# Performance work log

Measured on AMD Instinct MI355X. Metric: run time of the kernel, lower is better.

## Reference

```python
import jax, jax.numpy as jnp
import numpy as np
import math

B, T, D = 2, 2048, 1024
H = 16
DH = D // H  # 64
ROPE_BASE = 10000.0


def _rope_tables(seq_len, d_head, dtype=jnp.float32):
    inv_freq = 1.0 / (ROPE_BASE ** (jnp.arange(0, d_head, 2, dtype=jnp.float32) / d_head))
    pos = jnp.arange(seq_len, dtype=jnp.float32)
    freqs = jnp.outer(pos, inv_freq)            # [T, DH/2]
    emb = jnp.concatenate([freqs, freqs], -1)   # [T, DH]
    return jnp.cos(emb).astype(dtype), jnp.sin(emb).astype(dtype)


def _rotate_half(x):
    half = x.shape[-1] // 2
    return jnp.concatenate([-x[..., half:], x[..., :half]], axis=-1)


def setup_inputs() -> dict:
    key = jax.random.key(0)
    k1, k2, k3 = jax.random.split(key, 3)
    x = jax.random.normal(k1, (B, T, D), dtype=jnp.float32)
    qkv_w = jax.random.normal(k2, (D, 3 * D), dtype=jnp.float32) * (1.0 / math.sqrt(D))
    out_w = jax.random.normal(k3, (D, D), dtype=jnp.float32) * (1.0 / math.sqrt(D))
    out_b = jnp.zeros((D,), dtype=jnp.float32)
    mask = jnp.tril(jnp.ones((T, T), dtype=bool))[None, None]  # causal [1,1,T,T]
    return {"x": x, "mask": mask, "qkv_w": qkv_w, "out_w": out_w, "out_b": out_b}


def reference(x, mask, qkv_w, out_w, out_b):
    Bv, Tv, Dv = x.shape
    qkv = (x @ qkv_w).reshape(Bv, Tv, 3, H, DH)
    # [B, H, T, DH]
    q = jnp.transpose(qkv[:, :, 0], (0, 2, 1, 3))
    k = jnp.transpose(qkv[:, :, 1], (0, 2, 1, 3))
    v = jnp.transpose(qkv[:, :, 2], (0, 2, 1, 3))
    cos, sin = _rope_tables(Tv, DH, x.dtype)
    cos = cos[None, None]  # [1,1,T,DH]
    sin = sin[None, None]
    q = q * cos + _rotate_half(q) * sin
    k = k * cos + _rotate_half(k) * sin
    scores = jnp.einsum('bhqd,bhkd->bhqk', q, k) / math.sqrt(DH)
    scores = jnp.where(mask, scores, -jnp.inf)
    probs = jax.nn.softmax(scores, axis=-1)  # dropout = identity in eval mode
    out = jnp.einsum('bhqk,bhkd->bhqd', probs, v)
    out = jnp.transpose(out, (0, 2, 1, 3)).reshape(Bv, Tv, Dv)
    return out @ out_w + out_b
```

## Files before the change

### kernel.cpp

```cpp
#include <hip/hip_runtime.h>
#include <math.h>

typedef __attribute__((ext_vector_type(8))) short short8;
typedef __attribute__((ext_vector_type(4))) float f32x4;

static __device__ __forceinline__ unsigned short f2bf(float f) {
  unsigned u = __builtin_bit_cast(unsigned, f);
  u += 0x7fffu + ((u >> 16) & 1u);
  return (unsigned short)(u >> 16);
}
static __device__ __forceinline__ float bf2f(unsigned short h) {
  return __builtin_bit_cast(float, ((unsigned)h) << 16);
}
static __device__ __forceinline__ unsigned pack2bf(float a, float b) {
  return (unsigned)f2bf(a) | ((unsigned)f2bf(b) << 16);
}
static __device__ __forceinline__ unsigned pack2bf_t(float a, float b) {
  return __builtin_amdgcn_perm(__builtin_bit_cast(unsigned, b),
                               __builtin_bit_cast(unsigned, a), 0x07060302u);
}

typedef __attribute__((address_space(3))) unsigned short lds_us;
typedef __attribute__((address_space(1))) const unsigned short gbl_us;

static __device__ __forceinline__ void gld_lds16(const unsigned short* g,
                                                 unsigned short* l) {
  __builtin_amdgcn_global_load_lds((gbl_us*)g, (lds_us*)l, 16, 0, 0);
}

__global__ __launch_bounds__(256) void prep(const float* __restrict__ x,
                                            unsigned short* __restrict__ xb,
                                            const float* __restrict__ qkv_w,
                                            unsigned short* __restrict__ wqkvT,
                                            const float* __restrict__ out_w,
                                            unsigned short* __restrict__ woT) {
  __shared__ unsigned short T[64][68];
  const int blk = blockIdx.x;
  if (blk < 2048) {
    int i = (blk * 256 + threadIdx.x) * 8;
    float4 a = *(const float4*)(x + i);
    float4 b = *(const float4*)(x + i + 4);
    ushort4 u0 = {f2bf(a.x), f2bf(a.y), f2bf(a.z), f2bf(a.w)};
    ushort4 u1 = {f2bf(b.x), f2bf(b.y), f2bf(b.z), f2bf(b.w)};
    *(ushort4*)(xb + i) = u0;
    *(ushort4*)(xb + i + 4) = u1;
    return;
  }
  const float* in;
  unsigned short* out;
  int R, C, bx, by;
  if (blk < 2816) {
    in = qkv_w; out = wqkvT; R = 1024; C = 3072;
    bx = (blk - 2048) % 48; by = (blk - 2048) / 48;
  } else {
    in = out_w; out = woT; R = 1024; C = 1024;
    bx = (blk - 2816) % 16; by = (blk - 2816) / 16;
  }
  const int r0 = by * 64, c0 = bx * 64;
  const int tr = threadIdx.x >> 2;
  const int tc = (threadIdx.x & 3) * 16;
#pragma unroll
  for (int j = 0; j < 4; ++j) {
    float4 v = *(const float4*)(in + (size_t)(r0 + tr) * C + c0 + tc + j * 4);
    ushort4 u = {f2bf(v.x), f2bf(v.y), f2bf(v.z), f2bf(v.w)};
    *(ushort4*)&T[tr][tc + j * 4] = u;
  }
  __syncthreads();
  const int oc = tr;
#pragma unroll
  for (int g = 0; g < 4; ++g) {
    ushort4 u;
    u.x = T[tc + g * 4 + 0][oc];
    u.y = T[tc + g * 4 + 1][oc];
    u.z = T[tc + g * 4 + 2][oc];
    u.w = T[tc + g * 4 + 3][oc];
    *(ushort4*)(out + (size_t)(c0 + oc) * R + r0 + tc + g * 4) = u;
  }
}

__global__ __launch_bounds__(512) void gemm_qkv512(
    const unsigned short* __restrict__ A, const unsigned short* __restrict__ BT,
    unsigned short* __restrict__ qo, unsigned short* __restrict__ ko,
    unsigned short* __restrict__ vo) {
  __shared__ unsigned short As[2][4096];
  __shared__ unsigned short Bs[2][4096];
  const int tid = threadIdx.x;
  const int w = tid >> 6;
  const int lane = tid & 63;
  const int l15 = lane & 15;
  const int quad = lane >> 4;
  const int wm = w >> 2;
  const int wn = w & 3;
  const int m0 = blockIdx.y * 128;
  const int n0 = blockIdx.x * 128;

  f32x4 acc[4][2];
  const f32x4 zero4 = {0.f, 0.f, 0.f, 0.f};
#pragma unroll
  for (int mt = 0; mt < 4; ++mt)
#pragma unroll
    for (int nt = 0; nt < 2; ++nt) acc[mt][nt] = zero4;

  const int srow = tid >> 2;
  const int skch = (tid & 3) ^ ((srow >> 1) & 3);
  const int coff = tid * 8;
  const unsigned short* gA = A + (size_t)(m0 + srow) * 1024 + skch * 8;
  const unsigned short* gB = BT + (size_t)(n0 + srow) * 1024 + skch * 8;

  const int swz = (quad ^ ((l15 >> 1) & 3)) * 8;
  int aoff[4], boff[2];
#pragma unroll
  for (int t = 0; t < 4; ++t)
    aoff[t] = (wm * 64 + t * 16 + l15) * 32 + swz;
#pragma unroll
  for (int t = 0; t < 2; ++t)
    boff[t] = ((wn >> 1) * 64 + (wn & 1) * 16 + t * 32 + l15) * 32 + swz;

  auto issue = [&](int k0, int buf) {
    gld_lds16(gA + k0, &As[buf][coff]);
    gld_lds16(gB + k0, &Bs[buf][coff]);
  };

  issue(0, 0);
  for (int it = 0; it < 32; ++it) {
    const int cur = it & 1;
    __syncthreads();
    if (it + 1 < 32) issue((it + 1) * 32, cur ^ 1);

    short8 af[4], bf[2];
#pragma unroll
    for (int t = 0; t < 4; ++t) af[t] = *(const short8*)(&As[cur][aoff[t]]);
#pragma unroll
    for (int t = 0; t < 2; ++t) bf[t] = *(const short8*)(&Bs[cur][boff[t]]);
#pragma unroll
    for (int mt = 0; mt < 4; ++mt)
#pragma unroll
      for (int nt = 0; nt < 2; ++nt)
        acc[mt][nt] =
            __builtin_amdgcn_mfma_f32_16x16x32_bf16(af[mt], bf[nt], acc[mt][nt], 0, 0, 0);
  }

  const int b = m0 >> 11;
  const int ngrp = n0 + (wn >> 1) * 64;
  const int which = ngrp >> 10;
  const int h = (ngrp & 1023) >> 6;
  const int bh = b * 16 + h;
  if (which < 2) {
    unsigned short* dst = which ? ko : qo;
    const float qs = (which == 0) ? 0.1803368801111f : 1.0f;
    const int p = (wn & 1) * 16 + l15;
    float inv = __builtin_amdgcn_exp2f((float)p * -0.41524101186f) *
                0.15915494309f;
#pragma unroll
    for (int mt = 0; mt < 4; ++mt)
#pragma unroll
      for (int r = 0; r < 4; ++r) {
        int t = (m0 + wm * 64 + mt * 16 + quad * 4 + r) & 2047;
        float rv = __builtin_amdgcn_fractf((float)t * inv);
        float s = __builtin_amdgcn_sinf(rv);
        float c = __builtin_amdgcn_cosf(rv);
        float x0 = acc[mt][0][r], x1 = acc[mt][1][r];
        size_t rowoff = ((size_t)bh * 2048 + t) * 64;
        dst[rowoff + p]      = f2bf((x0 * c - x1 * s) * qs);
        dst[rowoff + p + 32] = f2bf((x1 * c + x0 * s) * qs);
      }
  } else {
#pragma unroll
    for (int mt = 0; mt < 4; ++mt) {
      int t0 = (m0 + wm * 64 + mt * 16 + quad * 4) & 2047;
#pragma unroll
      for (int nt = 0; nt < 2; ++nt) {
        int dh = (wn & 1) * 16 + nt * 32 + l15;
        ushort4 st = {f2bf(acc[mt][nt][0]), f2bf(acc[mt][nt][1]),
                      f2bf(acc[mt][nt][2]), f2bf(acc[mt][nt][3])};
        *(ushort4*)(vo + ((size_t)bh * 64 + dh) * 2048 + t0) = st;
      }
    }
  }
}

__global__ __launch_bounds__(256) void gemm_out(
    const unsigned short* __restrict__ A, const unsigned short* __restrict__ BT,
    const float* __restrict__ bias, float* __restrict__ out) {
  __shared__ unsigned short As[2][4096];
  __shared__ unsigned short Bs[2][2048];
  const int tid = threadIdx.x;
  const int w = tid >> 6;
  const int lane = tid & 63;
  const int l15 = lane & 15;
  const int quad = lane >> 4;
  const int wm = w >> 1, wn = w & 1;
  const int m0 = blockIdx.y * 128;
  const int n0 = blockIdx.x * 64;

  f32x4 acc[4][2];
  const f32x4 zero4 = {0.f, 0.f, 0.f, 0.f};
#pragma unroll
  for (int mt = 0; mt < 4; ++mt)
#pragma unroll
    for (int nt = 0; nt < 2; ++nt) acc[mt][nt] = zero4;

  int aco[2];
  const unsigned short* gA[2];
#pragma unroll
  for (int i = 0; i < 2; ++i) {
    int c = i * 256 + w * 64 + lane;
    int srow = c >> 2;
    int skch = (c & 3) ^ ((srow >> 1) & 3);
    aco[i] = c * 8;
    gA[i] = A + (size_t)(m0 + srow) * 1024 + skch * 8;
  }
  const int bc = w * 64 + lane;
  const int bsrow = bc >> 2;
  const int bskch = (bc & 3) ^ ((bsrow >> 1) & 3);
  const int bco = bc * 8;
  const unsigned short* gB = BT + (size_t)(n0 + bsrow) * 1024 + bskch * 8;

  const int swz = (quad ^ ((l15 >> 1) & 3)) * 8;
  int aoff[4], boff[2];
#pragma unroll
  for (int t = 0; t < 4; ++t) aoff[t] = (wm * 64 + t * 16 + l15) * 32 + swz;
#pragma unroll
  for (int t = 0; t < 2; ++t) boff[t] = (wn * 32 + t * 16 + l15) * 32 + swz;

  auto issue = [&](int k0, int buf) {
#pragma unroll
    for (int i = 0; i < 2; ++i) gld_lds16(gA[i] + k0, &As[buf][aco[i]]);
    gld_lds16(gB + k0, &Bs[buf][bco]);
  };

  issue(0, 0);
  for (int it = 0; it < 32; ++it) {
    const int cur = it & 1;
    __syncthreads();
    if (it + 1 < 32) issue((it + 1) * 32, cur ^ 1);

    short8 af[4], bf[2];
#pragma unroll
    for (int t = 0; t < 4; ++t) af[t] = *(const short8*)(&As[cur][aoff[t]]);
#pragma unroll
    for (int t = 0; t < 2; ++t) bf[t] = *(const short8*)(&Bs[cur][boff[t]]);
#pragma unroll
    for (int mt = 0; mt < 4; ++mt)
#pragma unroll
      for (int nt = 0; nt < 2; ++nt)
        acc[mt][nt] =
            __builtin_amdgcn_mfma_f32_16x16x32_bf16(af[mt], bf[nt], acc[mt][nt], 0, 0, 0);
  }

  const int nbase = n0 + wn * 32;
  float bv[2];
#pragma unroll
  for (int nt = 0; nt < 2; ++nt) bv[nt] = bias[nbase + nt * 16 + l15];
#pragma unroll
  for (int mt = 0; mt < 4; ++mt)
#pragma unroll
    for (int r = 0; r < 4; ++r) {
      int m = m0 + wm * 64 + mt * 16 + quad * 4 + r;
      float* orow = out + (size_t)m * 1024 + nbase + l15;
#pragma unroll
      for (int nt = 0; nt < 2; ++nt) orow[nt * 16] = acc[mt][nt][r] + bv[nt];
    }
}

__global__ __launch_bounds__(128, 4) void attn_mfma(
    const unsigned short* __restrict__ qg, const unsigned short* __restrict__ kg,
    const unsigned short* __restrict__ vtg, unsigned short* __restrict__ og,
    unsigned short* __restrict__ OpA,
    unsigned short* __restrict__ OpB,
    float* __restrict__ Lpart) {
  __shared__ unsigned short Ks[2][2048];
  __shared__ unsigned short Vt[2][2048];
  __shared__ unsigned short Ps[2][1024];
  const int bh = blockIdx.x;
  const int slot = blockIdx.y;
  int qb, chunk;
  if (slot < 32) {
    qb = 24 + (slot & 7);
    chunk = slot >> 3;
  } else if (slot < 56) {
    int s = slot - 32;
    qb = 16 + (s & 7);
    chunk = s >> 3;
  } else if (slot < 72) {
    int s = slot - 56;
    qb = 8 + (s & 7);
    chunk = s >> 3;
  } else {
    qb = slot - 72;
    chunk = 0;
  }
  const int n = qb >= 24 ? 4 : (qb >= 16 ? 3 : (qb >= 8 ? 2 : 1));
  const int t0 = chunk * 2 * (qb + 1) / n;
  const int t1 = (chunk + 1) * 2 * (qb + 1) / n;

  const int tid = threadIdx.x;
  const int w = tid >> 6;
  const int lane = tid & 63;
  const int l15 = lane & 15;
  const int quad = lane >> 4;
  const int m7 = l15 & 7;

  const int gq0 = qb * 64;
  const int qw = w * 32;

  short8 qf[2][2];
#pragma unroll
  for (int g = 0; g < 2; ++g) {
    const unsigned short* qrow =
        qg + ((size_t)bh * 2048 + gq0 + qw + g * 16 + l15) * 64;
    qf[g][0] = *(const short8*)(qrow + quad * 8);
    qf[g][1] = *(const short8*)(qrow + quad * 8 + 32);
  }

  f32x4 acc_o[2][4];
  f32x4 acc_l[2];
  const f32x4 zero4 = {0.f, 0.f, 0.f, 0.f};
#pragma unroll
  for (int g = 0; g < 2; ++g) {
    acc_l[g] = zero4;
#pragma unroll
    for (int nt = 0; nt < 4; ++nt) acc_o[g][nt] = zero4;
  }
  const short one_bf = (short)0x3F80;
  const short8 ones8 = {one_bf, one_bf, one_bf, one_bf,
                        one_bf, one_bf, one_bf, one_bf};

  const unsigned short* kbase = kg + (size_t)bh * 2048 * 64;
  const unsigned short* vtbase = vtg + (size_t)bh * 64 * 2048;
  unsigned short* pb = Ps[w];

  int doff[2], koff[2], voff[2];
#pragma unroll
  for (int i = 0; i < 2; ++i) {
    int d = i * 128 + tid;
    doff[i] = d * 8;
    int r = d >> 3;
    int lc = (d & 7) ^ (r & 7);
    koff[i] = r * 64 + lc * 8;
    int dh = (lc >> 2) * 32 + r;
    voff[i] = dh * 2048 + (lc & 3) * 8;
  }

  auto issue = [&](int kb, int buf) {
#pragma unroll
    for (int i = 0; i < 2; ++i) {
      gld_lds16(kbase + kb * 2048 + koff[i], &Ks[buf][doff[i]]);
      gld_lds16(vtbase + voff[i] + kb * 32, &Vt[buf][doff[i]]);
    }
  };

  const int kc0 = ((quad ^ m7) & 7) * 8;
  const int kc1 = kc0 ^ 32;
  int prd[2], vch[2];
#pragma unroll
  for (int g = 0; g < 2; ++g) prd[g] = l15 * 64 + (((g << 2) | quad) ^ m7) * 8;
#pragma unroll
  for (int h = 0; h < 2; ++h) vch[h] = (((h << 2) | quad) ^ m7) * 8;

  issue(t0, 0);
  for (int kb = t0; kb < t1; ++kb) {
    const int cur = (kb - t0) & 1;
    __syncthreads();
    if (kb + 1 < t1) issue(kb + 1, cur ^ 1);

    const unsigned short* kt = Ks[cur];
    const unsigned short* vt = Vt[cur];

    f32x4 s[2][2];
#pragma unroll
    for (int nt = 0; nt < 2; ++nt) {
      const unsigned short* kr = kt + (nt * 16 + l15) * 64;
      short8 kf0 = *(const short8*)(kr + kc0);
      short8 kf1 = *(const short8*)(kr + kc1);
#pragma unroll
      for (int g = 0; g < 2; ++g) {
        f32x4 cc = zero4;
        cc = __builtin_amdgcn_mfma_f32_16x16x32_bf16(kf0, qf[g][0], cc, 0, 0, 0);
        cc = __builtin_amdgcn_mfma_f32_16x16x32_bf16(kf1, qf[g][1], cc, 0, 0, 0);
        s[g][nt] = cc;
      }
    }

    if ((kb >> 1) == qb) {
#pragma unroll
      for (int g = 0; g < 2; ++g) {
        int gq = gq0 + qw + g * 16 + l15;
#pragma unroll
        for (int nt = 0; nt < 2; ++nt) {
          int gk = kb * 32 + nt * 16 + quad * 4;
#pragma unroll
          for (int r = 0; r < 4; ++r)
            if (gk + r > gq) s[g][nt][r] = -INFINITY;
        }
      }
    }

#pragma unroll
    for (int g = 0; g < 2; ++g)
#pragma unroll
      for (int nt = 0; nt < 2; ++nt) {
        float e0 = __builtin_amdgcn_exp2f(s[g][nt][0]);
        float e1 = __builtin_amdgcn_exp2f(s[g][nt][1]);
        float e2 = __builtin_amdgcn_exp2f(s[g][nt][2]);
        float e3 = __builtin_amdgcn_exp2f(s[g][nt][3]);
        int cidx = ((g << 2) | (nt * 2 + (quad >> 1))) ^ m7;
        uint2 pk;
        pk.x = pack2bf_t(e0, e1);
        pk.y = pack2bf_t(e2, e3);
        *(uint2*)&pb[l15 * 64 + cidx * 8 + (quad & 1) * 4] = pk;
      }

    short8 pfa = *(const short8*)&pb[prd[0]];
    short8 pfb = *(const short8*)&pb[prd[1]];

    acc_l[0] = __builtin_amdgcn_mfma_f32_16x16x32_bf16(ones8, pfa, acc_l[0], 0, 0, 0);
    acc_l[1] = __builtin_amdgcn_mfma_f32_16x16x32_bf16(ones8, pfb, acc_l[1], 0, 0, 0);

#pragma unroll
    for (int nt = 0; nt < 4; ++nt) {
      const unsigned short* vr = vt + ((nt & 1) * 16 + l15) * 64 + vch[nt >> 1];
      short8 vf = *(const short8*)vr;
      acc_o[0][nt] = __builtin_amdgcn_mfma_f32_16x16x32_bf16(vf, pfa, acc_o[0][nt], 0, 0, 0);
      acc_o[1][nt] = __builtin_amdgcn_mfma_f32_16x16x32_bf16(vf, pfb, acc_o[1][nt], 0, 0, 0);
    }
  }

  float lsum[2] = {acc_l[0][0], acc_l[1][0]};

  if (n == 1) {
    const int b = bh >> 4;
    const int h = bh & 15;
#pragma unroll
    for (int g = 0; g < 2; ++g) {
      float inv_l = 1.0f / lsum[g];
      unsigned short* orow =
          og + ((size_t)(b * 2048 + gq0 + qw + g * 16 + l15)) * 1024 + h * 64 +
          quad * 4;
#pragma unroll
      for (int nt = 0; nt < 4; ++nt) {
        *(unsigned*)(orow + nt * 16) =
            pack2bf(acc_o[g][nt][0] * inv_l, acc_o[g][nt][1] * inv_l);
        *(unsigned*)(orow + nt * 16 + 2) =
            pack2bf(acc_o[g][nt][2] * inv_l, acc_o[g][nt][3] * inv_l);
      }
    }
  } else {
    const int pidx = (qb < 16) ? (qb - 8) * 2 + chunk
                               : (qb < 24) ? 16 + (qb - 16) * 3 + chunk
                                           : 40 + (qb - 24) * 4 + chunk;
    unsigned short* obase = (pidx < 16)
                                ? OpB + ((size_t)(bh * 16 + pidx)) * 4096
                                : OpA + ((size_t)(bh * 56 + (pidx - 16))) * 4096;
#pragma unroll
    for (int g = 0; g < 2; ++g) {
      unsigned short* orow = obase + (qw + g * 16 + l15) * 64 + quad * 4;
#pragma unroll
      for (int nt = 0; nt < 4; ++nt) {
        *(unsigned*)(orow + nt * 16) = pack2bf(acc_o[g][nt][0], acc_o[g][nt][1]);
        *(unsigned*)(orow + nt * 16 + 2) = pack2bf(acc_o[g][nt][2], acc_o[g][nt][3]);
      }
      if (quad == 0)
        Lpart[(bh * 72 + pidx) * 64 + qw + g * 16 + l15] = lsum[g];
    }
  }
}

__global__ __launch_bounds__(256) void attn_combine(
    const unsigned short* __restrict__ OpA, const unsigned short* __restrict__ OpB,
    const float* __restrict__ Lpart, unsigned short* __restrict__ og) {
  int i = blockIdx.x * 256 + threadIdx.x;
  int dh = (i & 15) * 4;
  int q = (i >> 4) & 63;
  int idx = i >> 10;
  int bh = idx / 24;
  int qr = idx - bh * 24;
  int qb = 8 + qr;
  int count = qr < 8 ? 2 : (qr < 16 ? 3 : 4);
  int pstart = qr < 8 ? qr * 2 : (qr < 16 ? 16 + (qr - 8) * 3 : 40 + (qr - 16) * 4);
  float o0 = 0.f, o1 = 0.f, o2 = 0.f, o3 = 0.f, l = 0.f;
  for (int c = 0; c < count; ++c) {
    int pidx = pstart + c;
    const unsigned short* obase =
        (pidx < 16) ? OpB + ((size_t)(bh * 16 + pidx)) * 4096
                    : OpA + ((size_t)(bh * 56 + (pidx - 16))) * 4096;
    ushort4 a = *(const ushort4*)(obase + q * 64 + dh);
    o0 += bf2f(a.x);
    o1 += bf2f(a.y);
    o2 += bf2f(a.z);
    o3 += bf2f(a.w);
    l += Lpart[(bh * 72 + pidx) * 64 + q];
  }
  float inv = 1.0f / l;
  int bb = bh >> 4, h = bh & 15;
  int t = qb * 64 + q;
  unsigned short* orow = og + ((size_t)(bb * 2048 + t)) * 1024 + h * 64 + dh;
  *(unsigned*)(orow) = pack2bf(o0 * inv, o1 * inv);
  *(unsigned*)(orow + 2) = pack2bf(o2 * inv, o3 * inv);
}

extern "C" void kernel_launch(void* const* d_in, const int* in_sizes, int n_in,
                              void* d_out, int out_size, void* d_ws,
                              size_t ws_size, hipStream_t stream) {
  const float* x = (const float*)d_in[0];
  const float* qkv_w = (const float*)d_in[2];
  const float* out_w = (const float*)d_in[3];
  const float* out_b = (const float*)d_in[4];
  float* out = (float*)d_out;

  unsigned short* xb = (unsigned short*)d_ws;
  unsigned short* wqkvT = xb + 4194304;
  unsigned short* woT = wqkvT + 3145728;
  unsigned short* qb16 = woT + 1048576;
  unsigned short* kb16 = qb16 + 4194304;
  unsigned short* vt16 = kb16 + 4194304;
  unsigned short* ab = vt16 + 4194304;
  unsigned short* OpB = ab + 4194304;
  float* Lpart = (float*)(OpB + 4194304);
  unsigned short* OpA = xb;

  prep<<<3072, 256, 0, stream>>>(x, xb, qkv_w, wqkvT, out_w, woT);
  gemm_qkv512<<<dim3(24, 32), 512, 0, stream>>>(xb, wqkvT, qb16, kb16, vt16);
  attn_mfma<<<dim3(32, 80), 128, 0, stream>>>(qb16, kb16, vt16, ab, OpA, OpB,
                                              Lpart);
  attn_combine<<<3072, 256, 0, stream>>>(OpA, OpB, Lpart, ab);
  gemm_out<<<dim3(16, 32), 256, 0, stream>>>(ab, woT, out_b, out);
}
```

Baseline: 190.4 us.

## Load K/V tiles directly from global into registers, drop LDS staging and barriers

The attention kernel no longer stages K and V^T tiles through double-buffered shared memory with async global-to-LDS loads and a block-wide barrier each iteration. Each wave now loads its K fragments straight into registers, prefetching the next tile one iteration ahead, and loads V fragments directly from global at the top of each iteration. MFMA sections are wrapped in s_setprio raises, and launch bounds drop from 4 to 3 blocks per CU to allow more registers. This removes LDS traffic and __syncthreads, at the cost of redundant global/L2 reads across the waves of a block and exposed V load latency.

Measured after the change: 231.8 us. +21.7%, slower.

```diff
diff --git a/kernel.cpp b/kernel.cpp
--- a/kernel.cpp
+++ b/kernel.cpp
@@ -263,14 +263,12 @@
     }
 }
 
-__global__ __launch_bounds__(128, 4) void attn_mfma(
+__global__ __launch_bounds__(128, 3) void attn_mfma(
     const unsigned short* __restrict__ qg, const unsigned short* __restrict__ kg,
     const unsigned short* __restrict__ vtg, unsigned short* __restrict__ og,
     unsigned short* __restrict__ OpA,
     unsigned short* __restrict__ OpB,
     float* __restrict__ Lpart) {
-  __shared__ unsigned short Ks[2][2048];
-  __shared__ unsigned short Vt[2][2048];
   __shared__ unsigned short Ps[2][1024];
   const int bh = blockIdx.x;
   const int slot = blockIdx.y;
@@ -326,61 +324,49 @@
   const short8 ones8 = {one_bf, one_bf, one_bf, one_bf,
                         one_bf, one_bf, one_bf, one_bf};
 
-  const unsigned short* kbase = kg + (size_t)bh * 2048 * 64;
-  const unsigned short* vtbase = vtg + (size_t)bh * 64 * 2048;
+  const unsigned short* kp =
+      kg + (size_t)bh * 2048 * 64 + l15 * 64 + quad * 8;
+  const unsigned short* vp =
+      vtg + (size_t)bh * 64 * 2048 + (size_t)l15 * 2048 + quad * 8;
   unsigned short* pb = Ps[w];
 
-  int doff[2], koff[2], voff[2];
-#pragma unroll
-  for (int i = 0; i < 2; ++i) {
-    int d = i * 128 + tid;
-    doff[i] = d * 8;
-    int r = d >> 3;
-    int lc = (d & 7) ^ (r & 7);
-    koff[i] = r * 64 + lc * 8;
-    int dh = (lc >> 2) * 32 + r;
-    voff[i] = dh * 2048 + (lc & 3) * 8;
-  }
-
-  auto issue = [&](int kb, int buf) {
-#pragma unroll
-    for (int i = 0; i < 2; ++i) {
-      gld_lds16(kbase + kb * 2048 + koff[i], &Ks[buf][doff[i]]);
-      gld_lds16(vtbase + voff[i] + kb * 32, &Vt[buf][doff[i]]);
+  int prd[2];
+#pragma unroll
+  for (int g = 0; g < 2; ++g) prd[g] = l15 * 64 + (((g << 2) | quad) ^ m7) * 8;
+
+  auto loadK = [&](int kb, short8 (&kf)[2][2]) {
+    const unsigned short* p = kp + kb * 2048;
+#pragma unroll
+    for (int nt = 0; nt < 2; ++nt) {
+      kf[nt][0] = *(const short8*)(p + nt * 1024);
+      kf[nt][1] = *(const short8*)(p + nt * 1024 + 32);
     }
   };
 
-  const int kc0 = ((quad ^ m7) & 7) * 8;
-  const int kc1 = kc0 ^ 32;
-  int prd[2], vch[2];
-#pragma unroll
-  for (int g = 0; g < 2; ++g) prd[g] = l15 * 64 + (((g << 2) | quad) ^ m7) * 8;
-#pragma unroll
-  for (int h = 0; h < 2; ++h) vch[h] = (((h << 2) | quad) ^ m7) * 8;
-
-  issue(t0, 0);
+  short8 kf[2][2], kfn[2][2];
+  loadK(t0, kf);
+
   for (int kb = t0; kb < t1; ++kb) {
-    const int cur = (kb - t0) & 1;
-    __syncthreads();
-    if (kb + 1 < t1) issue(kb + 1, cur ^ 1);
-
-    const unsigned short* kt = Ks[cur];
-    const unsigned short* vt = Vt[cur];
+    short8 vf[4];
+#pragma unroll
+    for (int nt = 0; nt < 4; ++nt)
+      vf[nt] = *(const short8*)(vp + (size_t)nt * 32768 + kb * 32);
 
     f32x4 s[2][2];
+    __builtin_amdgcn_s_setprio(1);
 #pragma unroll
     for (int nt = 0; nt < 2; ++nt) {
-      const unsigned short* kr = kt + (nt * 16 + l15) * 64;
-      short8 kf0 = *(const short8*)(kr + kc0);
-      short8 kf1 = *(const short8*)(kr + kc1);
 #pragma unroll
       for (int g = 0; g < 2; ++g) {
         f32x4 cc = zero4;
-        cc = __builtin_amdgcn_mfma_f32_16x16x32_bf16(kf0, qf[g][0], cc, 0, 0, 0);
-        cc = __builtin_amdgcn_mfma_f32_16x16x32_bf16(kf1, qf[g][1], cc, 0, 0, 0);
+        cc = __builtin_amdgcn_mfma_f32_16x16x32_bf16(kf[nt][0], qf[g][0], cc, 0, 0, 0);
+        cc = __builtin_amdgcn_mfma_f32_16x16x32_bf16(kf[nt][1], qf[g][1], cc, 0, 0, 0);
         s[g][nt] = cc;
       }
     }
+    __builtin_amdgcn_s_setprio(0);
+
+    if (kb + 1 < t1) loadK(kb + 1, kfn);
 
     if ((kb >> 1) == qb) {
 #pragma unroll
@@ -414,15 +400,23 @@
     short8 pfa = *(const short8*)&pb[prd[0]];
     short8 pfb = *(const short8*)&pb[prd[1]];
 
+    __builtin_amdgcn_s_setprio(1);
     acc_l[0] = __builtin_amdgcn_mfma_f32_16x16x32_bf16(ones8, pfa, acc_l[0], 0, 0, 0);
     acc_l[1] = __builtin_amdgcn_mfma_f32_16x16x32_bf16(ones8, pfb, acc_l[1], 0, 0, 0);
 
 #pragma unroll
     for (int nt = 0; nt < 4; ++nt) {
-      const unsigned short* vr = vt + ((nt & 1) * 16 + l15) * 64 + vch[nt >> 1];
-      short8 vf = *(const short8*)vr;
-      acc_o[0][nt] = __builtin_amdgcn_mfma_f32_16x16x32_bf16(vf, pfa, acc_o[0][nt], 0, 0, 0);
-      acc_o[1][nt] = __builtin_amdgcn_mfma_f32_16x16x32_bf16(vf, pfb, acc_o[1][nt], 0, 0, 0);
+      acc_o[0][nt] = __builtin_amdgcn_mfma_f32_16x16x32_bf16(vf[nt], pfa, acc_o[0][nt], 0, 0, 0);
+      acc_o[1][nt] = __builtin_amdgcn_mfma_f32_16x16x32_bf16(vf[nt], pfb, acc_o[1][nt], 0, 0, 0);
+    }
+    __builtin_amdgcn_s_setprio(0);
+
+    if (kb + 1 < t1) {
+#pragma unroll
+      for (int nt = 0; nt < 2; ++nt) {
+        kf[nt][0] = kfn[nt][0];
+        kf[nt][1] = kfn[nt][1];
+      }
     }
   }
 
```

## Widen attention blocks to 128 queries with 4 waves and set MFMA priority

Applied to the files above, without the earlier changes.

The attention kernel now runs 256-thread blocks of four waves, so each block covers a 128-row query tile instead of 64. Each K/V tile staged in LDS is therefore shared by twice as many queries, and each thread issues one async load per tile instead of two. The split-K chunk scheduling, partial-output indexing and combine kernel are remapped to the new tile size. s_setprio hints are placed around the MFMA sections to favour matrix issue. The trade-offs are half as many blocks, which means less parallelism and coarser load balance, plus more LDS per block.

Measured after the change: 196.2 us. +3.1%, slower.

```diff
diff --git a/kernel.cpp b/kernel.cpp
--- a/kernel.cpp
+++ b/kernel.cpp
@@ -263,7 +263,7 @@
     }
 }
 
-__global__ __launch_bounds__(128, 4) void attn_mfma(
+__global__ __launch_bounds__(256, 4) void attn_mfma(
     const unsigned short* __restrict__ qg, const unsigned short* __restrict__ kg,
     const unsigned short* __restrict__ vtg, unsigned short* __restrict__ og,
     unsigned short* __restrict__ OpA,
@@ -271,28 +271,29 @@
     float* __restrict__ Lpart) {
   __shared__ unsigned short Ks[2][2048];
   __shared__ unsigned short Vt[2][2048];
-  __shared__ unsigned short Ps[2][1024];
+  __shared__ unsigned short Ps[4][1024];
   const int bh = blockIdx.x;
   const int slot = blockIdx.y;
-  int qb, chunk;
-  if (slot < 32) {
-    qb = 24 + (slot & 7);
-    chunk = slot >> 3;
-  } else if (slot < 56) {
-    int s = slot - 32;
-    qb = 16 + (s & 7);
-    chunk = s >> 3;
-  } else if (slot < 72) {
-    int s = slot - 56;
-    qb = 8 + (s & 7);
-    chunk = s >> 3;
+  int qb2, chunk;
+  if (slot < 16) {
+    qb2 = 12 + (slot & 3);
+    chunk = slot >> 2;
+  } else if (slot < 28) {
+    int s = slot - 16;
+    qb2 = 8 + (s & 3);
+    chunk = s >> 2;
+  } else if (slot < 36) {
+    int s = slot - 28;
+    qb2 = 4 + (s & 3);
+    chunk = s >> 2;
   } else {
-    qb = slot - 72;
+    qb2 = slot - 36;
     chunk = 0;
   }
-  const int n = qb >= 24 ? 4 : (qb >= 16 ? 3 : (qb >= 8 ? 2 : 1));
-  const int t0 = chunk * 2 * (qb + 1) / n;
-  const int t1 = (chunk + 1) * 2 * (qb + 1) / n;
+  const int n = qb2 >= 12 ? 4 : (qb2 >= 8 ? 3 : (qb2 >= 4 ? 2 : 1));
+  const int tt = 4 * (qb2 + 1);
+  const int t0 = chunk * tt / n;
+  const int t1 = (chunk + 1) * tt / n;
 
   const int tid = threadIdx.x;
   const int w = tid >> 6;
@@ -301,7 +302,7 @@
   const int quad = lane >> 4;
   const int m7 = l15 & 7;
 
-  const int gq0 = qb * 64;
+  const int gq0 = qb2 * 128;
   const int qw = w * 32;
 
   short8 qf[2][2];
@@ -330,24 +331,17 @@
   const unsigned short* vtbase = vtg + (size_t)bh * 64 * 2048;
   unsigned short* pb = Ps[w];
 
-  int doff[2], koff[2], voff[2];
-#pragma unroll
-  for (int i = 0; i < 2; ++i) {
-    int d = i * 128 + tid;
-    doff[i] = d * 8;
-    int r = d >> 3;
-    int lc = (d & 7) ^ (r & 7);
-    koff[i] = r * 64 + lc * 8;
-    int dh = (lc >> 2) * 32 + r;
-    voff[i] = dh * 2048 + (lc & 3) * 8;
-  }
+  const int d = tid;
+  const int doff = d * 8;
+  const int srow = d >> 3;
+  const int slc = (d & 7) ^ (srow & 7);
+  const int koff = srow * 64 + slc * 8;
+  const int sdh = (slc >> 2) * 32 + srow;
+  const int voff = sdh * 2048 + (slc & 3) * 8;
 
   auto issue = [&](int kb, int buf) {
-#pragma unroll
-    for (int i = 0; i < 2; ++i) {
-      gld_lds16(kbase + kb * 2048 + koff[i], &Ks[buf][doff[i]]);
-      gld_lds16(vtbase + voff[i] + kb * 32, &Vt[buf][doff[i]]);
-    }
+    gld_lds16(kbase + kb * 2048 + koff, &Ks[buf][doff]);
+    gld_lds16(vtbase + voff + kb * 32, &Vt[buf][doff]);
   };
 
   const int kc0 = ((quad ^ m7) & 7) * 8;
@@ -368,6 +362,7 @@
     const unsigned short* vt = Vt[cur];
 
     f32x4 s[2][2];
+    __builtin_amdgcn_s_setprio(1);
 #pragma unroll
     for (int nt = 0; nt < 2; ++nt) {
       const unsigned short* kr = kt + (nt * 16 + l15) * 64;
@@ -381,8 +376,9 @@
         s[g][nt] = cc;
       }
     }
-
-    if ((kb >> 1) == qb) {
+    __builtin_amdgcn_s_setprio(0);
+
+    if ((kb >> 2) == qb2) {
 #pragma unroll
       for (int g = 0; g < 2; ++g) {
         int gq = gq0 + qw + g * 16 + l15;
@@ -414,6 +410,7 @@
     short8 pfa = *(const short8*)&pb[prd[0]];
     short8 pfb = *(const short8*)&pb[prd[1]];
 
+    __builtin_amdgcn_s_setprio(1);
     acc_l[0] = __builtin_amdgcn_mfma_f32_16x16x32_bf16(ones8, pfa, acc_l[0], 0, 0, 0);
     acc_l[1] = __builtin_amdgcn_mfma_f32_16x16x32_bf16(ones8, pfb, acc_l[1], 0, 0, 0);
 
@@ -424,6 +421,7 @@
       acc_o[0][nt] = __builtin_amdgcn_mfma_f32_16x16x32_bf16(vf, pfa, acc_o[0][nt], 0, 0, 0);
       acc_o[1][nt] = __builtin_amdgcn_mfma_f32_16x16x32_bf16(vf, pfb, acc_o[1][nt], 0, 0, 0);
     }
+    __builtin_amdgcn_s_setprio(0);
   }
 
   float lsum[2] = {acc_l[0][0], acc_l[1][0]};
@@ -446,12 +444,12 @@
       }
     }
   } else {
-    const int pidx = (qb < 16) ? (qb - 8) * 2 + chunk
-                               : (qb < 24) ? 16 + (qb - 16) * 3 + chunk
-                                           : 40 + (qb - 24) * 4 + chunk;
-    unsigned short* obase = (pidx < 16)
-                                ? OpB + ((size_t)(bh * 16 + pidx)) * 4096
-                                : OpA + ((size_t)(bh * 56 + (pidx - 16))) * 4096;
+    const int pidx = (qb2 < 8) ? (qb2 - 4) * 2 + chunk
+                               : (qb2 < 12) ? 8 + (qb2 - 8) * 3 + chunk
+                                            : 20 + (qb2 - 12) * 4 + chunk;
+    unsigned short* obase =
+        (pidx < 16) ? OpB + ((size_t)(bh * 16 + pidx)) * 8192
+                    : OpA + ((size_t)(bh * 20 + (pidx - 16))) * 8192;
 #pragma unroll
     for (int g = 0; g < 2; ++g) {
       unsigned short* orow = obase + (qw + g * 16 + l15) * 64 + quad * 4;
@@ -461,7 +459,7 @@
         *(unsigned*)(orow + nt * 16 + 2) = pack2bf(acc_o[g][nt][2], acc_o[g][nt][3]);
       }
       if (quad == 0)
-        Lpart[(bh * 72 + pidx) * 64 + qw + g * 16 + l15] = lsum[g];
+        Lpart[(bh * 36 + pidx) * 128 + qw + g * 16 + l15] = lsum[g];
     }
   }
 }
@@ -471,29 +469,29 @@
     const float* __restrict__ Lpart, unsigned short* __restrict__ og) {
   int i = blockIdx.x * 256 + threadIdx.x;
   int dh = (i & 15) * 4;
-  int q = (i >> 4) & 63;
-  int idx = i >> 10;
-  int bh = idx / 24;
-  int qr = idx - bh * 24;
-  int qb = 8 + qr;
-  int count = qr < 8 ? 2 : (qr < 16 ? 3 : 4);
-  int pstart = qr < 8 ? qr * 2 : (qr < 16 ? 16 + (qr - 8) * 3 : 40 + (qr - 16) * 4);
+  int q = (i >> 4) & 127;
+  int idx = i >> 11;
+  int bh = idx / 12;
+  int qr = idx - bh * 12;
+  int qb2 = 4 + qr;
+  int count = qr < 4 ? 2 : (qr < 8 ? 3 : 4);
+  int pstart = qr < 4 ? qr * 2 : (qr < 8 ? 8 + (qr - 4) * 3 : 20 + (qr - 8) * 4);
   float o0 = 0.f, o1 = 0.f, o2 = 0.f, o3 = 0.f, l = 0.f;
   for (int c = 0; c < count; ++c) {
     int pidx = pstart + c;
     const unsigned short* obase =
-        (pidx < 16) ? OpB + ((size_t)(bh * 16 + pidx)) * 4096
-                    : OpA + ((size_t)(bh * 56 + (pidx - 16))) * 4096;
+        (pidx < 16) ? OpB + ((size_t)(bh * 16 + pidx)) * 8192
+                    : OpA + ((size_t)(bh * 20 + (pidx - 16))) * 8192;
     ushort4 a = *(const ushort4*)(obase + q * 64 + dh);
     o0 += bf2f(a.x);
     o1 += bf2f(a.y);
     o2 += bf2f(a.z);
     o3 += bf2f(a.w);
-    l += Lpart[(bh * 72 + pidx) * 64 + q];
+    l += Lpart[(bh * 36 + pidx) * 128 + q];
   }
   float inv = 1.0f / l;
   int bb = bh >> 4, h = bh & 15;
-  int t = qb * 64 + q;
+  int t = qb2 * 128 + q;
   unsigned short* orow = og + ((size_t)(bb * 2048 + t)) * 1024 + h * 64 + dh;
   *(unsigned*)(orow) = pack2bf(o0 * inv, o1 * inv);
   *(unsigned*)(orow + 2) = pack2bf(o2 * inv, o3 * inv);
@@ -521,7 +519,7 @@
 
   prep<<<3072, 256, 0, stream>>>(x, xb, qkv_w, wqkvT, out_w, woT);
   gemm_qkv512<<<dim3(24, 32), 512, 0, stream>>>(xb, wqkvT, qb16, kb16, vt16);
-  attn_mfma<<<dim3(32, 80), 128, 0, stream>>>(qb16, kb16, vt16, ab, OpA, OpB,
+  attn_mfma<<<dim3(32, 40), 256, 0, stream>>>(qb16, kb16, vt16, ab, OpA, OpB,
                                               Lpart);
   attn_combine<<<3072, 256, 0, stream>>>(OpA, OpB, Lpart, ab);
   gemm_out<<<dim3(16, 32), 256, 0, stream>>>(ab, woT, out_b, out);
```

## Widen output GEMM tile to 128x128 with 512 threads; add MFMA priority hints in attention

Applied to the files above, without the earlier changes.

The output projection GEMM now runs 8 waves per block on a 128x128 tile instead of 4 waves on a 128x64 tile, halving the grid. Each thread loads one A chunk and one B chunk per K step, and the wave-to-column mapping is interleaved. The aim is more reuse of the A tile and fewer redundant A loads, at the cost of fewer blocks (256) across the CUs. Separately, the attention loop raises wave priority around its MFMA sections with s_setprio, so the matrix work is favoured over other waves' softmax and LDS work.

New measurement: 187.7 us (median of 2 runs). Within noise of the previous version (-1.4%).

```diff
diff --git a/kernel.cpp b/kernel.cpp
--- a/kernel.cpp
+++ b/kernel.cpp
@@ -179,19 +179,20 @@
   }
 }
 
-__global__ __launch_bounds__(256) void gemm_out(
+__global__ __launch_bounds__(512) void gemm_out(
     const unsigned short* __restrict__ A, const unsigned short* __restrict__ BT,
     const float* __restrict__ bias, float* __restrict__ out) {
   __shared__ unsigned short As[2][4096];
-  __shared__ unsigned short Bs[2][2048];
+  __shared__ unsigned short Bs[2][4096];
   const int tid = threadIdx.x;
   const int w = tid >> 6;
   const int lane = tid & 63;
   const int l15 = lane & 15;
   const int quad = lane >> 4;
-  const int wm = w >> 1, wn = w & 1;
+  const int wm = w >> 2;
+  const int wn = w & 3;
   const int m0 = blockIdx.y * 128;
-  const int n0 = blockIdx.x * 64;
+  const int n0 = blockIdx.x * 128;
 
   f32x4 acc[4][2];
   const f32x4 zero4 = {0.f, 0.f, 0.f, 0.f};
@@ -200,33 +201,24 @@
 #pragma unroll
     for (int nt = 0; nt < 2; ++nt) acc[mt][nt] = zero4;
 
-  int aco[2];
-  const unsigned short* gA[2];
-#pragma unroll
-  for (int i = 0; i < 2; ++i) {
-    int c = i * 256 + w * 64 + lane;
-    int srow = c >> 2;
-    int skch = (c & 3) ^ ((srow >> 1) & 3);
-    aco[i] = c * 8;
-    gA[i] = A + (size_t)(m0 + srow) * 1024 + skch * 8;
-  }
-  const int bc = w * 64 + lane;
-  const int bsrow = bc >> 2;
-  const int bskch = (bc & 3) ^ ((bsrow >> 1) & 3);
-  const int bco = bc * 8;
-  const unsigned short* gB = BT + (size_t)(n0 + bsrow) * 1024 + bskch * 8;
+  const int srow = tid >> 2;
+  const int skch = (tid & 3) ^ ((srow >> 1) & 3);
+  const int coff = tid * 8;
+  const unsigned short* gA = A + (size_t)(m0 + srow) * 1024 + skch * 8;
+  const unsigned short* gB = BT + (size_t)(n0 + srow) * 1024 + skch * 8;
 
   const int swz = (quad ^ ((l15 >> 1) & 3)) * 8;
   int aoff[4], boff[2];
 #pragma unroll
-  for (int t = 0; t < 4; ++t) aoff[t] = (wm * 64 + t * 16 + l15) * 32 + swz;
-#pragma unroll
-  for (int t = 0; t < 2; ++t) boff[t] = (wn * 32 + t * 16 + l15) * 32 + swz;
+  for (int t = 0; t < 4; ++t)
+    aoff[t] = (wm * 64 + t * 16 + l15) * 32 + swz;
+#pragma unroll
+  for (int t = 0; t < 2; ++t)
+    boff[t] = ((wn >> 1) * 64 + (wn & 1) * 16 + t * 32 + l15) * 32 + swz;
 
   auto issue = [&](int k0, int buf) {
-#pragma unroll
-    for (int i = 0; i < 2; ++i) gld_lds16(gA[i] + k0, &As[buf][aco[i]]);
-    gld_lds16(gB + k0, &Bs[buf][bco]);
+    gld_lds16(gA + k0, &As[buf][coff]);
+    gld_lds16(gB + k0, &Bs[buf][coff]);
   };
 
   issue(0, 0);
@@ -248,18 +240,18 @@
             __builtin_amdgcn_mfma_f32_16x16x32_bf16(af[mt], bf[nt], acc[mt][nt], 0, 0, 0);
   }
 
-  const int nbase = n0 + wn * 32;
+  const int nb2 = n0 + (wn >> 1) * 64 + (wn & 1) * 16;
   float bv[2];
 #pragma unroll
-  for (int nt = 0; nt < 2; ++nt) bv[nt] = bias[nbase + nt * 16 + l15];
+  for (int nt = 0; nt < 2; ++nt) bv[nt] = bias[nb2 + nt * 32 + l15];
 #pragma unroll
   for (int mt = 0; mt < 4; ++mt)
 #pragma unroll
     for (int r = 0; r < 4; ++r) {
       int m = m0 + wm * 64 + mt * 16 + quad * 4 + r;
-      float* orow = out + (size_t)m * 1024 + nbase + l15;
-#pragma unroll
-      for (int nt = 0; nt < 2; ++nt) orow[nt * 16] = acc[mt][nt][r] + bv[nt];
+      float* orow = out + (size_t)m * 1024 + nb2 + l15;
+      orow[0]  = acc[mt][0][r] + bv[0];
+      orow[32] = acc[mt][1][r] + bv[1];
     }
 }
 
@@ -368,6 +360,7 @@
     const unsigned short* vt = Vt[cur];
 
     f32x4 s[2][2];
+    __builtin_amdgcn_s_setprio(1);
 #pragma unroll
     for (int nt = 0; nt < 2; ++nt) {
       const unsigned short* kr = kt + (nt * 16 + l15) * 64;
@@ -381,6 +374,7 @@
         s[g][nt] = cc;
       }
     }
+    __builtin_amdgcn_s_setprio(0);
 
     if ((kb >> 1) == qb) {
 #pragma unroll
@@ -414,6 +408,7 @@
     short8 pfa = *(const short8*)&pb[prd[0]];
     short8 pfb = *(const short8*)&pb[prd[1]];
 
+    __builtin_amdgcn_s_setprio(1);
     acc_l[0] = __builtin_amdgcn_mfma_f32_16x16x32_bf16(ones8, pfa, acc_l[0], 0, 0, 0);
     acc_l[1] = __builtin_amdgcn_mfma_f32_16x16x32_bf16(ones8, pfb, acc_l[1], 0, 0, 0);
 
@@ -424,6 +419,7 @@
       acc_o[0][nt] = __builtin_amdgcn_mfma_f32_16x16x32_bf16(vf, pfa, acc_o[0][nt], 0, 0, 0);
       acc_o[1][nt] = __builtin_amdgcn_mfma_f32_16x16x32_bf16(vf, pfb, acc_o[1][nt], 0, 0, 0);
     }
+    __builtin_amdgcn_s_setprio(0);
   }
 
   float lsum[2] = {acc_l[0][0], acc_l[1][0]};
@@ -524,5 +520,5 @@
   attn_mfma<<<dim3(32, 80), 128, 0, stream>>>(qb16, kb16, vt16, ab, OpA, OpB,
                                               Lpart);
   attn_combine<<<3072, 256, 0, stream>>>(OpA, OpB, Lpart, ab);
-  gemm_out<<<dim3(16, 32), 256, 0, stream>>>(ab, woT, out_b, out);
-}
+  gemm_out<<<dim3(8, 32), 512, 0, stream>>>(ab, woT, out_b, out);
+}
```
